# Performance work log

Measured on AMD Instinct MI355X. Metric: run time of the kernel, lower is better.

The kernel has to match this reference:

```python
import jax, jax.numpy as jnp
import numpy as np

HH, WW = 7, 7  # pooled output size (module init: height, width)


def setup_inputs() -> dict:
    key = jax.random.key(0)
    k1, k2, k3, k4, k5 = jax.random.split(key, 5)
    C, Hf, Wf = 512, 64, 256        # conv feature map (stride 8)
    B = 4096                        # number of RoI boxes
    img_h, img_w = 512, 2048        # original image size
    feats = jax.random.normal(k1, (C, Hf, Wf), dtype=jnp.float32)
    w = jax.random.uniform(k2, (B,), minval=16.0, maxval=256.0)
    h = jax.random.uniform(k3, (B,), minval=16.0, maxval=128.0)
    xc = jax.random.uniform(k4, (B,), minval=0.0, maxval=float(img_w))
    yc = jax.random.uniform(k5, (B,), minval=0.0, maxval=float(img_h))
    boxes = jnp.stack([xc, yc, w, h], axis=1).astype(jnp.float32)  # (B,4) xc,yc,w,h in image coords
    return {"feats": feats, "boxes": boxes, "img_height": img_h, "img_width": img_w}


def _bilinear_sample(feats, px, py):
    """feats: (C,Hf,Wf); px,py: (B,HH,WW) pixel coords in feature map. Zero padding outside."""
    C, Hf, Wf = feats.shape
    x0 = jnp.floor(px)
    y0 = jnp.floor(py)
    x1 = x0 + 1.0
    y1 = y0 + 1.0
    wx1 = px - x0
    wx0 = 1.0 - wx1
    wy1 = py - y0
    wy0 = 1.0 - wy1

    def gather(xi, yi):
        valid = (xi >= 0) & (xi <= Wf - 1) & (yi >= 0) & (yi <= Hf - 1)
        xi_c = jnp.clip(xi, 0, Wf - 1).astype(jnp.int32)
        yi_c = jnp.clip(yi, 0, Hf - 1).astype(jnp.int32)
        v = feats[:, yi_c, xi_c]                     # (C,B,HH,WW)
        return v * valid[None].astype(feats.dtype)

    out = (gather(x0, y0) * (wx0 * wy0)[None]
           + gather(x1, y0) * (wx1 * wy0)[None]
           + gather(x0, y1) * (wx0 * wy1)[None]
           + gather(x1, y1) * (wx1 * wy1)[None])    # (C,B,HH,WW)
    return jnp.transpose(out, (1, 0, 2, 3))          # (B,C,HH,WW)


def reference(feats, boxes, img_height, img_width):
    # box_to_affine (densecap BoxToAffine, align_corners=True normalization) fused
    # with affine_grid: sample coords computed inline per box.
    B = boxes.shape[0]
    C, Hf, Wf = feats.shape
    xc, yc, w, h = boxes[:, 0], boxes[:, 1], boxes[:, 2], boxes[:, 3]
    tx = jnp.linspace(-1.0, 1.0, WW, dtype=feats.dtype)
    ty = jnp.linspace(-1.0, 1.0, HH, dtype=feats.dtype)
    inv_w = 1.0 / (img_width - 1)
    inv_h = 1.0 / (img_height - 1)
    # normalized image coords: gx = (2*xc-(W-1))/(W-1) + tx * w/(W-1)
    gx = (2.0 * xc[:, None] - (img_width - 1)) * inv_w + (w * inv_w)[:, None] * tx[None, :]   # (B,WW)
    gy = (2.0 * yc[:, None] - (img_height - 1)) * inv_h + (h * inv_h)[:, None] * ty[None, :]  # (B,HH)
    # map normalized [-1,1] to feature-map pixel coords (align_corners=True)
    px = (gx + 1.0) * 0.5 * (Wf - 1)
    py = (gy + 1.0) * 0.5 * (Hf - 1)
    px = jnp.broadcast_to(px[:, None, :], (B, HH, WW))
    py = jnp.broadcast_to(py[:, :, None], (B, HH, WW))
    return _bilinear_sample(feats, px, py)            # (B,C,HH,WW)
```

## Files before the change

kernel.cpp:

```cpp
#include <hip/hip_runtime.h>
#include <math.h>

#define HH 7
#define WW 7
#define CC 512
#define HF 64
#define WF 256
#define NS 49
#define TILE_PAD 260
#define NE4 ((256 * NS) / 4)

typedef float floatv4 __attribute__((ext_vector_type(4)));

__global__ __launch_bounds__(256) void transpose_feats(const float* __restrict__ in,
                                                       float* __restrict__ out) {
    __shared__ float tile[32][33];
    const int P = HF * WF;
    int p  = blockIdx.x * 32 + threadIdx.x;
    int cb = blockIdx.y * 32;
#pragma unroll
    for (int r = 0; r < 32; r += 8)
        tile[threadIdx.y + r][threadIdx.x] = in[(size_t)(cb + threadIdx.y + r) * P + p];
    __syncthreads();
    int c  = cb + threadIdx.x;
    int pb = blockIdx.x * 32;
#pragma unroll
    for (int r = 0; r < 32; r += 8)
        out[(size_t)(pb + threadIdx.y + r) * CC + c] = tile[threadIdx.x][threadIdx.y + r];
}

__device__ __forceinline__ void box_setup(int s, int b,
                                          const float* __restrict__ boxes,
                                          const int* __restrict__ ih_p,
                                          const int* __restrict__ iw_p,
                                          int4* o_out, float4* w_out) {
    int i = s / WW;
    int j = s - i * WW;
    float IW1 = (float)(iw_p[0] - 1);
    float IH1 = (float)(ih_p[0] - 1);
    float xc = boxes[b * 4 + 0];
    float yc = boxes[b * 4 + 1];
    float bw = boxes[b * 4 + 2];
    float bh = boxes[b * 4 + 3];
    float inv_w = 1.0f / IW1;
    float inv_h = 1.0f / IH1;
    float tx = (float)(j - 3) * (1.0f / 3.0f);
    float ty = (float)(i - 3) * (1.0f / 3.0f);
    float gx = (2.0f * xc - IW1) * inv_w + (bw * inv_w) * tx;
    float gy = (2.0f * yc - IH1) * inv_h + (bh * inv_h) * ty;
    float px = (gx + 1.0f) * 0.5f * (float)(WF - 1);
    float py = (gy + 1.0f) * 0.5f * (float)(HF - 1);

    float x0f = floorf(px), y0f = floorf(py);
    float wx1 = px - x0f, wx0 = 1.0f - wx1;
    float wy1 = py - y0f, wy0 = 1.0f - wy1;
    float x1f = x0f + 1.0f, y1f = y0f + 1.0f;

    bool vx0 = (x0f >= 0.0f) && (x0f <= (float)(WF - 1));
    bool vx1 = (x1f >= 0.0f) && (x1f <= (float)(WF - 1));
    bool vy0 = (y0f >= 0.0f) && (y0f <= (float)(HF - 1));
    bool vy1 = (y1f >= 0.0f) && (y1f <= (float)(HF - 1));

    int xi0 = (int)fminf(fmaxf(x0f, 0.0f), (float)(WF - 1));
    int xi1 = (int)fminf(fmaxf(x1f, 0.0f), (float)(WF - 1));
    int yi0 = (int)fminf(fmaxf(y0f, 0.0f), (float)(HF - 1));
    int yi1 = (int)fminf(fmaxf(y1f, 0.0f), (float)(HF - 1));

    int4 o;
    o.x = yi0 * WF + xi0;
    o.y = yi0 * WF + xi1;
    o.z = yi1 * WF + xi0;
    o.w = yi1 * WF + xi1;
    float4 w4;
    w4.x = wx0 * wy0 * ((vx0 && vy0) ? 1.0f : 0.0f);
    w4.y = wx1 * wy0 * ((vx1 && vy0) ? 1.0f : 0.0f);
    w4.z = wx0 * wy1 * ((vx0 && vy1) ? 1.0f : 0.0f);
    w4.w = wx1 * wy1 * ((vx1 && vy1) ? 1.0f : 0.0f);
    *o_out = o;
    *w_out = w4;
}

__global__ __launch_bounds__(256) void roi_pool_v2(const float* __restrict__ src,
                                                   const float* __restrict__ boxes,
                                                   const int* __restrict__ ih_p,
                                                   const int* __restrict__ iw_p,
                                                   float* __restrict__ out) {
    __shared__ int4   s_off[NS];
    __shared__ float4 s_wt[NS];
    __shared__ float  tile[NS * TILE_PAD];

    const int b   = blockIdx.x;
    const int tid = threadIdx.x;
    const int g   = tid & 63;
    const int sp  = tid >> 6;

    if (tid < NS) {
        int4 o; float4 w4;
        box_setup(tid, b, boxes, ih_p, iw_p, &o, &w4);
        o.x *= (CC / 4); o.y *= (CC / 4); o.z *= (CC / 4); o.w *= (CC / 4);
        s_off[tid] = o;
        s_wt[tid]  = w4;
    }
    __syncthreads();

    const size_t outbase = (size_t)b * (CC * NS);

    for (int c0 = 0; c0 < CC; c0 += 256) {
        const float4* src4 = (const float4*)(src + c0);
        for (int s = sp; s < NS; s += 4) {
            int4   o = s_off[s];
            float4 w = s_wt[s];
            float4 a = src4[o.x + g];
            float4 bb = src4[o.y + g];
            float4 c = src4[o.z + g];
            float4 d = src4[o.w + g];
            float4 v;
            v.x = a.x * w.x + bb.x * w.y + c.x * w.z + d.x * w.w;
            v.y = a.y * w.x + bb.y * w.y + c.y * w.z + d.y * w.w;
            v.z = a.z * w.x + bb.z * w.y + c.z * w.z + d.z * w.w;
            v.w = a.w * w.x + bb.w * w.y + c.w * w.z + d.w * w.w;
            *(float4*)(&tile[s * TILE_PAD + 4 * g]) = v;
        }
        __syncthreads();
        float* outc = out + outbase + (size_t)c0 * NS;
#pragma unroll 4
        for (int k4 = tid; k4 < NE4; k4 += 256) {
            int e = k4 * 4;
            int c = e / NS;
            int s = e - c * NS;
            floatv4 v;
            v.x = tile[s * TILE_PAD + c];
            if (++s == NS) { s = 0; ++c; }
            v.y = tile[s * TILE_PAD + c];
            if (++s == NS) { s = 0; ++c; }
            v.z = tile[s * TILE_PAD + c];
            if (++s == NS) { s = 0; ++c; }
            v.w = tile[s * TILE_PAD + c];
            __builtin_nontemporal_store(v, (floatv4*)outc + k4);
        }
        __syncthreads();
    }
}

__global__ __launch_bounds__(256) void roi_pool_fb(const float* __restrict__ src,
                                                   const float* __restrict__ boxes,
                                                   const int* __restrict__ ih_p,
                                                   const int* __restrict__ iw_p,
                                                   float* __restrict__ out) {
    __shared__ int4   s_off[NS];
    __shared__ float4 s_wt[NS];
    __shared__ float  tile[NS * 257];

    const int b   = blockIdx.x;
    const int tid = threadIdx.x;

    if (tid < NS) {
        int4 o; float4 w4;
        box_setup(tid, b, boxes, ih_p, iw_p, &o, &w4);
        s_off[tid] = o;
        s_wt[tid]  = w4;
    }
    __syncthreads();

    const size_t outbase = (size_t)b * (CC * NS);
    for (int c0 = 0; c0 < CC; c0 += 256) {
        const int cterm = (c0 + tid) * (HF * WF);
        for (int s = 0; s < NS; ++s) {
            int4   o = s_off[s];
            float4 w = s_wt[s];
            float v = src[o.x + cterm] * w.x + src[o.y + cterm] * w.y +
                      src[o.z + cterm] * w.z + src[o.w + cterm] * w.w;
            tile[s * 257 + tid] = v;
        }
        __syncthreads();
        const size_t ob = outbase + (size_t)c0 * NS;
        for (int k = tid; k < 256 * NS; k += 256) {
            int cl = k / NS;
            int s  = k - cl * NS;
            out[ob + k] = tile[s * 257 + cl];
        }
        __syncthreads();
    }
}

extern "C" void kernel_launch(void* const* d_in, const int* in_sizes, int n_in,
                              void* d_out, int out_size, void* d_ws, size_t ws_size,
                              hipStream_t stream) {
    const float* feats = (const float*)d_in[0];
    const float* boxes = (const float*)d_in[1];
    const int*   ih    = (const int*)d_in[2];
    const int*   iw    = (const int*)d_in[3];
    float*       out   = (float*)d_out;
    const int B = in_sizes[1] / 4;

    const size_t need = (size_t)CC * HF * WF * sizeof(float);
    if (ws_size >= need) {
        float* tf = (float*)d_ws;
        dim3 tb(32, 8);
        dim3 tg((HF * WF) / 32, CC / 32);
        transpose_feats<<<tg, tb, 0, stream>>>(feats, tf);
        roi_pool_v2<<<B, 256, 0, stream>>>(tf, boxes, ih, iw, out);
    } else {
        roi_pool_fb<<<B, 256, 0, stream>>>(feats, boxes, ih, iw, out);
    }
}
```

Before: 537.9 us.

## Shrink channel chunk to 128 with XOR-swizzled smem tile and register-cached offsets

The pooling kernel now processes channels in chunks of 128 instead of 256, which cuts the shared tile from about 51KB to 32KB so more blocks can be resident per CU. Each box's sample offsets and weights are cached in registers once rather than re-read from shared memory every chunk. The tile is stored channel-major with an XOR swizzle on the sample index to avoid bank conflicts on both the scalar writes and the transposed reads. In exchange there are twice as many chunk iterations and barriers, more index arithmetic per element, and higher register use.

```diff
diff --git a/kernel.cpp b/kernel.cpp
--- a/kernel.cpp
+++ b/kernel.cpp
@@ -7,8 +7,9 @@
 #define HF 64
 #define WF 256
 #define NS 49
-#define TILE_PAD 260
-#define NE4 ((256 * NS) / 4)
+#define CHUNK 128
+#define ROWS4 (CC / 4)
+#define NE4 ((CHUNK * NS) / 4)
 
 typedef float floatv4 __attribute__((ext_vector_type(4)));
 
@@ -80,62 +81,79 @@
     *w_out = w4;
 }
 
-__global__ __launch_bounds__(256) void roi_pool_v2(const float* __restrict__ src,
+__global__ __launch_bounds__(256) void roi_pool_v3(const float* __restrict__ src,
                                                    const float* __restrict__ boxes,
                                                    const int* __restrict__ ih_p,
                                                    const int* __restrict__ iw_p,
                                                    float* __restrict__ out) {
     __shared__ int4   s_off[NS];
     __shared__ float4 s_wt[NS];
-    __shared__ float  tile[NS * TILE_PAD];
+    __shared__ float  tile[CHUNK * 64];
 
     const int b   = blockIdx.x;
     const int tid = threadIdx.x;
-    const int g   = tid & 63;
-    const int sp  = tid >> 6;
+    const int g   = tid & 31;
+    const int h   = tid >> 5;
 
     if (tid < NS) {
         int4 o; float4 w4;
         box_setup(tid, b, boxes, ih_p, iw_p, &o, &w4);
-        o.x *= (CC / 4); o.y *= (CC / 4); o.z *= (CC / 4); o.w *= (CC / 4);
+        o.x *= ROWS4; o.y *= ROWS4; o.z *= ROWS4; o.w *= ROWS4;
         s_off[tid] = o;
         s_wt[tid]  = w4;
     }
     __syncthreads();
 
+    int4   o_r[7];
+    float4 w_r[7];
+    int    sig_r[7];
+#pragma unroll
+    for (int it = 0; it < 7; ++it) {
+        int s = h + (it << 3);
+        if (s < NS) {
+            o_r[it]   = s_off[s];
+            w_r[it]   = s_wt[s];
+            sig_r[it] = (s >> 2) | ((s & 3) << 4);
+        }
+    }
+
     const size_t outbase = (size_t)b * (CC * NS);
-
-    for (int c0 = 0; c0 < CC; c0 += 256) {
-        const float4* src4 = (const float4*)(src + c0);
-        for (int s = sp; s < NS; s += 4) {
-            int4   o = s_off[s];
-            float4 w = s_wt[s];
-            float4 a = src4[o.x + g];
-            float4 bb = src4[o.y + g];
-            float4 c = src4[o.z + g];
-            float4 d = src4[o.w + g];
-            float4 v;
-            v.x = a.x * w.x + bb.x * w.y + c.x * w.z + d.x * w.w;
-            v.y = a.y * w.x + bb.y * w.y + c.y * w.z + d.y * w.w;
-            v.z = a.z * w.x + bb.z * w.y + c.z * w.z + d.z * w.w;
-            v.w = a.w * w.x + bb.w * w.y + c.w * w.z + d.w * w.w;
-            *(float4*)(&tile[s * TILE_PAD + 4 * g]) = v;
+    const float4* src4   = (const float4*)src;
+
+    for (int c0 = 0; c0 < CC; c0 += CHUNK) {
+        const int cb4 = c0 >> 2;
+#pragma unroll
+        for (int it = 0; it < 7; ++it) {
+            int s = h + (it << 3);
+            if (s < NS) {
+                int4   o = o_r[it];
+                float4 w = w_r[it];
+                float4 a  = src4[o.x + cb4 + g];
+                float4 bb = src4[o.y + cb4 + g];
+                float4 c  = src4[o.z + cb4 + g];
+                float4 d  = src4[o.w + cb4 + g];
+                int base = g << 8;
+                int sw   = sig_r[it] ^ g;
+                tile[base +       sw] = a.x * w.x + bb.x * w.y + c.x * w.z + d.x * w.w;
+                tile[base +  64 + sw] = a.y * w.x + bb.y * w.y + c.y * w.z + d.y * w.w;
+                tile[base + 128 + sw] = a.z * w.x + bb.z * w.y + c.z * w.z + d.z * w.w;
+                tile[base + 192 + sw] = a.w * w.x + bb.w * w.y + c.w * w.z + d.w * w.w;
+            }
         }
         __syncthreads();
         float* outc = out + outbase + (size_t)c0 * NS;
-#pragma unroll 4
         for (int k4 = tid; k4 < NE4; k4 += 256) {
-            int e = k4 * 4;
+            int e = k4 << 2;
             int c = e / NS;
             int s = e - c * NS;
             floatv4 v;
-            v.x = tile[s * TILE_PAD + c];
+            v.x = tile[(c << 6) + (((s >> 2) | ((s & 3) << 4)) ^ (c >> 2))];
             if (++s == NS) { s = 0; ++c; }
-            v.y = tile[s * TILE_PAD + c];
+            v.y = tile[(c << 6) + (((s >> 2) | ((s & 3) << 4)) ^ (c >> 2))];
             if (++s == NS) { s = 0; ++c; }
-            v.z = tile[s * TILE_PAD + c];
+            v.z = tile[(c << 6) + (((s >> 2) | ((s & 3) << 4)) ^ (c >> 2))];
             if (++s == NS) { s = 0; ++c; }
-            v.w = tile[s * TILE_PAD + c];
+            v.w = tile[(c << 6) + (((s >> 2) | ((s & 3) << 4)) ^ (c >> 2))];
             __builtin_nontemporal_store(v, (floatv4*)outc + k4);
         }
         __syncthreads();
@@ -199,7 +217,7 @@
         dim3 tb(32, 8);
         dim3 tg((HF * WF) / 32, CC / 32);
         transpose_feats<<<tg, tb, 0, stream>>>(feats, tf);
-        roi_pool_v2<<<B, 256, 0, stream>>>(tf, boxes, ih, iw, out);
+        roi_pool_v3<<<B, 256, 0, stream>>>(tf, boxes, ih, iw, out);
     } else {
         roi_pool_fb<<<B, 256, 0, stream>>>(feats, boxes, ih, iw, out);
     }
```

New measurement: 537.4 us. Within noise of the previous version (-0.1%).
